# Optimization experiments

Hardware: AMD Instinct MI355X
Metric: run time of the kernel (lower is better)

Reference implementation:

```python
import jax, jax.numpy as jnp
import numpy as np

E = 256      # embedding_dim
H = 8        # num_heads
D = E // H   # head_dim = 32
F = 1024     # dim_feedforward
EPS = 1e-5


def layer_norm(x, gamma, beta):
    mu = jnp.mean(x, axis=-1, keepdims=True)
    var = jnp.var(x, axis=-1, keepdims=True)
    return (x - mu) * jax.lax.rsqrt(var + EPS) * gamma + beta


def setup_inputs() -> dict:
    key = jax.random.key(0)
    ks = jax.random.split(key, 12)
    s = lambda fan_in: 1.0 / np.sqrt(fan_in)
    src = jax.random.normal(ks[0], (4, 2048, E), dtype=jnp.float32)
    w_in = jax.random.uniform(ks[1], (3 * E, E), minval=-s(E), maxval=s(E), dtype=jnp.float32)
    w_out = jax.random.uniform(ks[2], (E, E), minval=-s(E), maxval=s(E), dtype=jnp.float32)
    w1 = jax.random.uniform(ks[3], (F, E), minval=-s(E), maxval=s(E), dtype=jnp.float32)
    b1 = jax.random.uniform(ks[4], (F,), minval=-s(E), maxval=s(E), dtype=jnp.float32)
    w2 = jax.random.uniform(ks[5], (E, F), minval=-s(F), maxval=s(F), dtype=jnp.float32)
    b2 = jax.random.uniform(ks[6], (E,), minval=-s(F), maxval=s(F), dtype=jnp.float32)
    g1 = jnp.ones((E,), jnp.float32)
    beta1 = jnp.zeros((E,), jnp.float32)
    g2 = jnp.ones((E,), jnp.float32)
    beta2 = jnp.zeros((E,), jnp.float32)
    return {"src": src, "w_in": w_in, "w_out": w_out, "w1": w1, "b1": b1,
            "w2": w2, "b2": b2, "g1": g1, "beta1": beta1, "g2": g2, "beta2": beta2}


def reference(src, w_in, w_out, w1, b1, w2, b2, g1, beta1, g2, beta2):
    B, S, _ = src.shape
    scale = D ** (-0.5)
    # --- pre-norm self-attention block ---
    x = layer_norm(src, g1, beta1)                 # [B,S,E]
    qkv = x @ w_in.T                               # [B,S,3E]
    q, k, v = jnp.split(qkv, 3, axis=-1)
    q = q.reshape(B, S, H, D).transpose(0, 2, 1, 3)  # [B,H,S,D]
    k = k.reshape(B, S, H, D).transpose(0, 2, 1, 3)
    v = v.reshape(B, S, H, D).transpose(0, 2, 1, 3)
    scores = jnp.einsum('bhqd,bhkd->bhqk', q, k) * scale  # [B,H,S,S]
    attn = jax.nn.softmax(scores, axis=-1)
    out = jnp.einsum('bhqk,bhkd->bhqd', attn, v)   # [B,H,S,D]
    out = out.transpose(0, 2, 1, 3).reshape(B, S, E)
    src = src + out @ w_out.T
    # --- pre-norm FFN block ---
    y = layer_norm(src, g2, beta2)
    y = jax.nn.relu(y @ w1.T + b1) @ w2.T + b2
    return src + y
```

## Files before the change

### kernel.cpp

```cpp
#include <hip/hip_runtime.h>
#include <hip/hip_bf16.h>
#include <math.h>

typedef unsigned short u16;
typedef unsigned int   u32;
using bf16x8 = __attribute__((ext_vector_type(8))) short;
using f32x4  = __attribute__((ext_vector_type(4))) float;

#define TE 256
#define TH 8
#define TS 2048
#define TB 4
#define NTOK 8192
#define QSCALE 0.2550120651552454f
#define EXP2(x) __builtin_amdgcn_exp2f(x)

__device__ __forceinline__ void async16(const u16* g, u16* l) {
    __builtin_amdgcn_global_load_lds(
        (const __attribute__((address_space(1))) u32*)g,
        (__attribute__((address_space(3))) u32*)l, 16, 0, 0);
}
__device__ __forceinline__ u32 pkbf(float a, float b) {
    u32 ua = __float_as_uint(a) + 0x8000u;
    u32 ub = __float_as_uint(b) + 0x8000u;
    return __builtin_amdgcn_perm(ub, ua, 0x07060302u);
}

__global__ __launch_bounds__(256) void ln_bf(const float* __restrict__ in,
        u16* __restrict__ out, const float* __restrict__ gamma,
        const float* __restrict__ beta) {
    int row  = blockIdx.x * 4 + (threadIdx.x >> 6);
    int lane = threadIdx.x & 63;
    float4 v = ((const float4*)(in + (size_t)row * TE))[lane];
    float s  = v.x + v.y + v.z + v.w;
    float s2 = v.x*v.x + v.y*v.y + v.z*v.z + v.w*v.w;
    #pragma unroll
    for (int off = 32; off > 0; off >>= 1) {
        s  += __shfl_down(s,  off, 64);
        s2 += __shfl_down(s2, off, 64);
    }
    s  = __shfl(s,  0, 64);
    s2 = __shfl(s2, 0, 64);
    float mu = s * (1.f / TE);
    float rs = rsqrtf(s2 * (1.f / TE) - mu * mu + 1e-5f);
    float4 g = ((const float4*)gamma)[lane];
    float4 b = ((const float4*)beta )[lane];
    u32 lo = pkbf((v.x - mu) * rs * g.x + b.x, (v.y - mu) * rs * g.y + b.y);
    u32 hi = pkbf((v.z - mu) * rs * g.z + b.z, (v.w - mu) * rs * g.w + b.w);
    ((uint2*)(out + (size_t)row * TE))[lane] = make_uint2(lo, hi);
}

__global__ __launch_bounds__(256) void convw(const float* __restrict__ s0, u16* d0,
        const float* __restrict__ s1, u16* d1, const float* __restrict__ s2, u16* d2,
        const float* __restrict__ s3, u16* d3) {
    int i = (blockIdx.x * 256 + threadIdx.x) * 4;
    const float* s; u16* d;
    if      (i < 196608) { s = s0; d = d0; }
    else if (i < 262144) { s = s1; d = d1; i -= 196608; }
    else if (i < 524288) { s = s2; d = d2; i -= 262144; }
    else                 { s = s3; d = d3; i -= 524288; }
    float4 v = *(const float4*)(s + i);
    *(uint2*)(d + i) = make_uint2(pkbf(v.x, v.y), pkbf(v.z, v.w));
}

template<int K, int BM, int EPI>
__global__ __launch_bounds__(256) void mgemm(const u16* __restrict__ A,
        const u16* __restrict__ W, const float* __restrict__ bias,
        const float* __restrict__ R, float* __restrict__ Cf,
        u16* __restrict__ Cb, int M) {
    constexpr int BN = BM;
    __shared__ u16 Al[2][BM * 32];
    __shared__ u16 Wl[2][BN * 32];
    const int tid = threadIdx.x, w = tid >> 6, l = tid & 63;
    const int n0 = blockIdx.y * BM;
    const int m0 = blockIdx.x * BN;
    constexpr int NT = (BM == 128) ? 4 : 2;
    constexpr int NF = (BM == 128) ? 4 : 2;
    const int tw = (w & 1) * NT * 16;
    const int fw = (w >> 1) * NF * 16;
    const int fr = l & 15, fq = l >> 4;
    const int sr = l >> 2, sc = (l & 3) * 8;
    f32x4 acc[NT][NF];
    #pragma unroll
    for (int t = 0; t < NT; t++)
        #pragma unroll
        for (int f = 0; f < NF; f++)
            #pragma unroll
            for (int r = 0; r < 4; r++) acc[t][f][r] = 0.f;

    for (int k0 = 0; k0 < K; k0 += 64) {
        __syncthreads();
        #pragma unroll
        for (int hh = 0; hh < 2; hh++) {
            const int kc = k0 + hh * 32;
            if (BM == 128) {
                #pragma unroll
                for (int c = 0; c < 2; c++) {
                    int rr = (w * 2 + c) * 16 + sr;
                    async16(A + (size_t)(n0 + rr) * K + kc + sc, &Al[hh][(w * 2 + c) * 512]);
                    async16(W + (size_t)(m0 + rr) * K + kc + sc, &Wl[hh][(w * 2 + c) * 512]);
                }
            } else {
                int rr = w * 16 + sr;
                async16(A + (size_t)(n0 + rr) * K + kc + sc, &Al[hh][w * 512]);
                async16(W + (size_t)(m0 + rr) * K + kc + sc, &Wl[hh][w * 512]);
            }
        }
        __syncthreads();
        #pragma unroll
        for (int hh = 0; hh < 2; hh++) {
            bf16x8 af[NT], wf[NF];
            #pragma unroll
            for (int t = 0; t < NT; t++)
                af[t] = *(const bf16x8*)&Al[hh][(tw + t * 16 + fr) * 32 + fq * 8];
            #pragma unroll
            for (int f = 0; f < NF; f++)
                wf[f] = *(const bf16x8*)&Wl[hh][(fw + f * 16 + fr) * 32 + fq * 8];
            #pragma unroll
            for (int t = 0; t < NT; t++)
                #pragma unroll
                for (int f = 0; f < NF; f++)
                    acc[t][f] = __builtin_amdgcn_mfma_f32_16x16x32_bf16(
                        wf[f], af[t], acc[t][f], 0, 0, 0);
        }
    }
    #pragma unroll
    for (int t = 0; t < NT; t++) {
        const int tok = n0 + tw + t * 16 + fr;
        #pragma unroll
        for (int f = 0; f < NF; f++) {
            const int fb = m0 + fw + f * 16 + fq * 4;
            f32x4 v = acc[t][f];
            if (EPI == 0) {
                const float qs = (fb < 256) ? QSCALE : 1.f;
                *(uint2*)(Cb + (size_t)tok * M + fb) =
                    make_uint2(pkbf(v[0]*qs, v[1]*qs), pkbf(v[2]*qs, v[3]*qs));
            } else if (EPI == 1) {
                float4 r4 = *(const float4*)(R + (size_t)tok * M + fb);
                *(float4*)(Cf + (size_t)tok * M + fb) =
                    make_float4(v[0]+r4.x, v[1]+r4.y, v[2]+r4.z, v[3]+r4.w);
            } else if (EPI == 2) {
                float4 b4 = *(const float4*)(bias + fb);
                *(uint2*)(Cb + (size_t)tok * M + fb) = make_uint2(
                    pkbf(fmaxf(v[0]+b4.x, 0.f), fmaxf(v[1]+b4.y, 0.f)),
                    pkbf(fmaxf(v[2]+b4.z, 0.f), fmaxf(v[3]+b4.w, 0.f)));
            } else {
                float4 b4 = *(const float4*)(bias + fb);
                float4 r4 = *(const float4*)(R + (size_t)tok * M + fb);
                *(float4*)(Cf + (size_t)tok * M + fb) = make_float4(
                    v[0]+b4.x+r4.x, v[1]+b4.y+r4.y, v[2]+b4.z+r4.z, v[3]+b4.w+r4.w);
            }
        }
    }
}

__global__ __launch_bounds__(256) void attn_k(const u16* __restrict__ qkv,
        u16* __restrict__ attn) {
    const int bh = blockIdx.x, b = bh >> 3, h = bh & 7;
    const int q0 = blockIdx.y * 64;
    const int tid = threadIdx.x, w = tid >> 6, l = tid & 63;
    const int qw = w & 1, kw = w >> 1;
    const int fr = l & 15, fq = l >> 4;
    const size_t btok = (size_t)b * TS;

    __shared__ u16 Vt[2][4 * 1296];
    __shared__ u16 Pl[4][32 * 40];

    bf16x8 qf[2];
    #pragma unroll
    for (int qs = 0; qs < 2; qs++)
        qf[qs] = *(const bf16x8*)(qkv +
            (btok + q0 + qw * 32 + qs * 16 + fr) * 768 + h * 32 + fq * 8);

    f32x4 o[2][2];
    #pragma unroll
    for (int ds = 0; ds < 2; ds++)
        #pragma unroll
        for (int qs = 0; qs < 2; qs++)
            #pragma unroll
            for (int r = 0; r < 4; r++) o[ds][qs][r] = 0.f;
    float ps[2] = {0.f, 0.f};

    u16* Pw = Pl[w];
    const int vkv = l * 2, vd0 = qw * 16;
    const u16* kbase = qkv + btok * 768 + 256 + h * 32;
    const int kvbase = kw * 1024;

    for (int it = 0; it < 8; it++) {
        const int kv0 = kvbase + it * 128;
        __syncthreads();
        {
            const u16* va = qkv + (btok + kv0 + vkv) * 768 + 512 + h * 32 + vd0;
            uint4 ra0 = *(const uint4*)va;
            uint4 ra1 = *(const uint4*)(va + 8);
            uint4 rb0 = *(const uint4*)(va + 768);
            uint4 rb1 = *(const uint4*)(va + 776);
            const u16* pa0 = (const u16*)&ra0; const u16* pa1 = (const u16*)&ra1;
            const u16* pb0 = (const u16*)&rb0; const u16* pb1 = (const u16*)&rb1;
            u16* vb_ = &Vt[kw][(vkv >> 5) * 1296 + (vkv & 31)];
            #pragma unroll
            for (int i = 0; i < 8; i++) {
                *(u32*)&vb_[(vd0 + i) * 40]     = (u32)pa0[i] | ((u32)pb0[i] << 16);
                *(u32*)&vb_[(vd0 + 8 + i) * 40] = (u32)pa1[i] | ((u32)pb1[i] << 16);
            }
        }
        __syncthreads();
        #pragma unroll
        for (int sub = 0; sub < 4; sub++) {
            const u16* krow = kbase + (size_t)(kv0 + sub * 32) * 768;
            bf16x8 kf0 = *(const bf16x8*)(krow + (size_t)fr * 768 + fq * 8);
            bf16x8 kf1 = *(const bf16x8*)(krow + (size_t)(16 + fr) * 768 + fq * 8);
            f32x4 z; z[0] = z[1] = z[2] = z[3] = 0.f;
            #pragma unroll
            for (int qs = 0; qs < 2; qs++) {
                f32x4 st0 = __builtin_amdgcn_mfma_f32_16x16x32_bf16(kf0, qf[qs], z, 0, 0, 0);
                f32x4 st1 = __builtin_amdgcn_mfma_f32_16x16x32_bf16(kf1, qf[qs], z, 0, 0, 0);
                float p0[4], p1[4];
                #pragma unroll
                for (int r = 0; r < 4; r++) { p0[r] = EXP2(st0[r]); p1[r] = EXP2(st1[r]); }
                ps[qs] += ((p0[0]+p0[1]) + (p0[2]+p0[3]))
                        + ((p1[0]+p1[1]) + (p1[2]+p1[3]));
                u16* prow = &Pw[(qs * 16 + fr) * 40];
                *(uint2*)&prow[fq * 4]      = make_uint2(pkbf(p0[0],p0[1]), pkbf(p0[2],p0[3]));
                *(uint2*)&prow[16 + fq * 4] = make_uint2(pkbf(p1[0],p1[1]), pkbf(p1[2],p1[3]));
            }
            bf16x8 pf0 = *(const bf16x8*)&Pw[fr * 40 + fq * 8];
            bf16x8 pf1 = *(const bf16x8*)&Pw[(16 + fr) * 40 + fq * 8];
            bf16x8 vf0 = *(const bf16x8*)&Vt[kw][sub * 1296 + fr * 40 + fq * 8];
            bf16x8 vf1 = *(const bf16x8*)&Vt[kw][sub * 1296 + (16 + fr) * 40 + fq * 8];
            o[0][0] = __builtin_amdgcn_mfma_f32_16x16x32_bf16(vf0, pf0, o[0][0], 0, 0, 0);
            o[0][1] = __builtin_amdgcn_mfma_f32_16x16x32_bf16(vf0, pf1, o[0][1], 0, 0, 0);
            o[1][0] = __builtin_amdgcn_mfma_f32_16x16x32_bf16(vf1, pf0, o[1][0], 0, 0, 0);
            o[1][1] = __builtin_amdgcn_mfma_f32_16x16x32_bf16(vf1, pf1, o[1][1], 0, 0, 0);
        }
    }
    #pragma unroll
    for (int qs = 0; qs < 2; qs++) {
        ps[qs] += __shfl_xor(ps[qs], 16, 64);
        ps[qs] += __shfl_xor(ps[qs], 32, 64);
    }
    __syncthreads();
    float* mrg = (float*)&Vt[0][0];
    if (kw == 1) {
        float* p = mrg + (qw * 64 + l) * 18;
        #pragma unroll
        for (int ds = 0; ds < 2; ds++)
            #pragma unroll
            for (int qs = 0; qs < 2; qs++)
                #pragma unroll
                for (int r = 0; r < 4; r++) p[ds * 8 + qs * 4 + r] = o[ds][qs][r];
        p[16] = ps[0]; p[17] = ps[1];
    }
    __syncthreads();
    if (kw == 0) {
        const float* p = mrg + (qw * 64 + l) * 18;
        #pragma unroll
        for (int ds = 0; ds < 2; ds++)
            #pragma unroll
            for (int qs = 0; qs < 2; qs++)
                #pragma unroll
                for (int r = 0; r < 4; r++) o[ds][qs][r] += p[ds * 8 + qs * 4 + r];
        ps[0] += p[16]; ps[1] += p[17];
        #pragma unroll
        for (int qs = 0; qs < 2; qs++) {
            float inv = 1.f / ps[qs];
            int tok = (int)btok + q0 + qw * 32 + qs * 16 + fr;
            #pragma unroll
            for (int ds = 0; ds < 2; ds++) {
                *(uint2*)(attn + (size_t)tok * 256 + h * 32 + ds * 16 + fq * 4) =
                    make_uint2(pkbf(o[ds][qs][0]*inv, o[ds][qs][1]*inv),
                               pkbf(o[ds][qs][2]*inv, o[ds][qs][3]*inv));
            }
        }
    }
}

extern "C" void kernel_launch(void* const* d_in, const int* in_sizes, int n_in,
                              void* d_out, int out_size, void* d_ws, size_t ws_size,
                              hipStream_t stream) {
    const float* src  = (const float*)d_in[0];
    const float* w_in = (const float*)d_in[1];
    const float* w_out= (const float*)d_in[2];
    const float* w1   = (const float*)d_in[3];
    const float* b1   = (const float*)d_in[4];
    const float* w2   = (const float*)d_in[5];
    const float* b2   = (const float*)d_in[6];
    const float* g1   = (const float*)d_in[7];
    const float* be1  = (const float*)d_in[8];
    const float* g2   = (const float*)d_in[9];
    const float* be2  = (const float*)d_in[10];
    float* out = (float*)d_out;

    u16* xb    = (u16*)d_ws;
    u16* qkvb  = xb + (size_t)NTOK * 256;
    u16* attnb = xb;
    u16* h1b   = (u16*)d_ws;
    u16* x2b   = (u16*)((char*)d_ws + (size_t)NTOK * 1024 * 2);
    u16* wib   = x2b + (size_t)NTOK * 256;
    u16* wob   = wib + 768 * 256;
    u16* w1b   = wob + 256 * 256;
    u16* w2b   = w1b + 1024 * 256;

    convw<<<768, 256, 0, stream>>>(w_in, wib, w_out, wob, w1, w1b, w2, w2b);
    ln_bf<<<NTOK / 4, 256, 0, stream>>>(src, xb, g1, be1);
    mgemm<256, 128, 0><<<dim3(6, 64), 256, 0, stream>>>(
        xb, wib, nullptr, nullptr, nullptr, qkvb, 768);
    attn_k<<<dim3(32, 32), 256, 0, stream>>>(qkvb, attnb);
    mgemm<256, 64, 1><<<dim3(4, 128), 256, 0, stream>>>(
        attnb, wob, nullptr, src, out, nullptr, 256);
    ln_bf<<<NTOK / 4, 256, 0, stream>>>(out, x2b, g2, be2);
    mgemm<256, 128, 2><<<dim3(8, 64), 256, 0, stream>>>(
        x2b, w1b, b1, nullptr, nullptr, h1b, 1024);
    mgemm<1024, 64, 3><<<dim3(4, 128), 256, 0, stream>>>(
        h1b, w2b, b2, out, out, nullptr, 256);
}
```

Baseline: 196.2 us.

## Emit V transposed from QKV GEMM and rewrite attention with 32x32 MFMA

The QKV GEMM epilogue now writes Q and K into a 512-wide buffer and scatters V into a per-head transposed [bh][d][seq] layout. This removes the in-kernel LDS transpose of V and the related barriers in attention. The attention kernel switches to 32x32x16 MFMAs and keeps P in registers through cvt_pk_bf16 and permlane32_swap instead of an LDS round trip. It also remaps the block index so that blocks sharing a head are spread across the grid. The trade-off is that the epilogue's scalar, strided 2-byte V stores are uncoalesced, which may slow the GEMM.

```diff
diff --git a/kernel.cpp b/kernel.cpp
--- a/kernel.cpp
+++ b/kernel.cpp
@@ -6,6 +6,8 @@
 typedef unsigned int   u32;
 using bf16x8 = __attribute__((ext_vector_type(8))) short;
 using f32x4  = __attribute__((ext_vector_type(4))) float;
+using f32x16 = __attribute__((ext_vector_type(16))) float;
+using u32v4  = __attribute__((ext_vector_type(4))) u32;
 
 #define TE 256
 #define TH 8
@@ -24,6 +26,9 @@
     u32 ua = __float_as_uint(a) + 0x8000u;
     u32 ub = __float_as_uint(b) + 0x8000u;
     return __builtin_amdgcn_perm(ub, ua, 0x07060302u);
+}
+__device__ __forceinline__ u16 bf1(float a) {
+    return (u16)((__float_as_uint(a) + 0x8000u) >> 16);
 }
 
 __global__ __launch_bounds__(256) void ln_bf(const float* __restrict__ in,
@@ -132,9 +137,19 @@
             const int fb = m0 + fw + f * 16 + fq * 4;
             f32x4 v = acc[t][f];
             if (EPI == 0) {
-                const float qs = (fb < 256) ? QSCALE : 1.f;
-                *(uint2*)(Cb + (size_t)tok * M + fb) =
-                    make_uint2(pkbf(v[0]*qs, v[1]*qs), pkbf(v[2]*qs, v[3]*qs));
+                if (fb < 512) {
+                    const float qs = (fb < 256) ? QSCALE : 1.f;
+                    *(uint2*)(Cb + (size_t)tok * 512 + fb) =
+                        make_uint2(pkbf(v[0]*qs, v[1]*qs), pkbf(v[2]*qs, v[3]*qs));
+                } else {
+                    const int hh = (fb - 512) >> 5, dd = (fb - 512) & 31;
+                    u16* vt = (u16*)Cf +
+                        ((size_t)((tok >> 11) * 8 + hh) * 32 + dd) * 2048 + (tok & 2047);
+                    vt[0]    = bf1(v[0]);
+                    vt[2048] = bf1(v[1]);
+                    vt[4096] = bf1(v[2]);
+                    vt[6144] = bf1(v[3]);
+                }
             } else if (EPI == 1) {
                 float4 r4 = *(const float4*)(R + (size_t)tok * M + fb);
                 *(float4*)(Cf + (size_t)tok * M + fb) =
@@ -154,124 +169,85 @@
     }
 }
 
-__global__ __launch_bounds__(256) void attn_k(const u16* __restrict__ qkv,
-        u16* __restrict__ attn) {
-    const int bh = blockIdx.x, b = bh >> 3, h = bh & 7;
-    const int q0 = blockIdx.y * 64;
+__global__ __launch_bounds__(256, 4) void attn_k(const u16* __restrict__ qk,
+        const u16* __restrict__ vt, u16* __restrict__ attn) {
+    const int id = blockIdx.x;
+    const int bh   = (id & 7) * 4 + (id >> 8);
+    const int tile = (id >> 3) & 31;
+    const int b = bh >> 3, h = bh & 7;
     const int tid = threadIdx.x, w = tid >> 6, l = tid & 63;
     const int qw = w & 1, kw = w >> 1;
-    const int fr = l & 15, fq = l >> 4;
+    const int lq = l & 31, hi = l >> 5;
     const size_t btok = (size_t)b * TS;
-
-    __shared__ u16 Vt[2][4 * 1296];
-    __shared__ u16 Pl[4][32 * 40];
-
-    bf16x8 qf[2];
-    #pragma unroll
-    for (int qs = 0; qs < 2; qs++)
-        qf[qs] = *(const bf16x8*)(qkv +
-            (btok + q0 + qw * 32 + qs * 16 + fr) * 768 + h * 32 + fq * 8);
-
-    f32x4 o[2][2];
-    #pragma unroll
-    for (int ds = 0; ds < 2; ds++)
-        #pragma unroll
-        for (int qs = 0; qs < 2; qs++)
-            #pragma unroll
-            for (int r = 0; r < 4; r++) o[ds][qs][r] = 0.f;
-    float ps[2] = {0.f, 0.f};
-
-    u16* Pw = Pl[w];
-    const int vkv = l * 2, vd0 = qw * 16;
-    const u16* kbase = qkv + btok * 768 + 256 + h * 32;
-    const int kvbase = kw * 1024;
-
-    for (int it = 0; it < 8; it++) {
-        const int kv0 = kvbase + it * 128;
-        __syncthreads();
-        {
-            const u16* va = qkv + (btok + kv0 + vkv) * 768 + 512 + h * 32 + vd0;
-            uint4 ra0 = *(const uint4*)va;
-            uint4 ra1 = *(const uint4*)(va + 8);
-            uint4 rb0 = *(const uint4*)(va + 768);
-            uint4 rb1 = *(const uint4*)(va + 776);
-            const u16* pa0 = (const u16*)&ra0; const u16* pa1 = (const u16*)&ra1;
-            const u16* pb0 = (const u16*)&rb0; const u16* pb1 = (const u16*)&rb1;
-            u16* vb_ = &Vt[kw][(vkv >> 5) * 1296 + (vkv & 31)];
-            #pragma unroll
-            for (int i = 0; i < 8; i++) {
-                *(u32*)&vb_[(vd0 + i) * 40]     = (u32)pa0[i] | ((u32)pb0[i] << 16);
-                *(u32*)&vb_[(vd0 + 8 + i) * 40] = (u32)pa1[i] | ((u32)pb1[i] << 16);
-            }
-        }
-        __syncthreads();
-        #pragma unroll
-        for (int sub = 0; sub < 4; sub++) {
-            const u16* krow = kbase + (size_t)(kv0 + sub * 32) * 768;
-            bf16x8 kf0 = *(const bf16x8*)(krow + (size_t)fr * 768 + fq * 8);
-            bf16x8 kf1 = *(const bf16x8*)(krow + (size_t)(16 + fr) * 768 + fq * 8);
-            f32x4 z; z[0] = z[1] = z[2] = z[3] = 0.f;
-            #pragma unroll
-            for (int qs = 0; qs < 2; qs++) {
-                f32x4 st0 = __builtin_amdgcn_mfma_f32_16x16x32_bf16(kf0, qf[qs], z, 0, 0, 0);
-                f32x4 st1 = __builtin_amdgcn_mfma_f32_16x16x32_bf16(kf1, qf[qs], z, 0, 0, 0);
-                float p0[4], p1[4];
-                #pragma unroll
-                for (int r = 0; r < 4; r++) { p0[r] = EXP2(st0[r]); p1[r] = EXP2(st1[r]); }
-                ps[qs] += ((p0[0]+p0[1]) + (p0[2]+p0[3]))
-                        + ((p1[0]+p1[1]) + (p1[2]+p1[3]));
-                u16* prow = &Pw[(qs * 16 + fr) * 40];
-                *(uint2*)&prow[fq * 4]      = make_uint2(pkbf(p0[0],p0[1]), pkbf(p0[2],p0[3]));
-                *(uint2*)&prow[16 + fq * 4] = make_uint2(pkbf(p1[0],p1[1]), pkbf(p1[2],p1[3]));
-            }
-            bf16x8 pf0 = *(const bf16x8*)&Pw[fr * 40 + fq * 8];
-            bf16x8 pf1 = *(const bf16x8*)&Pw[(16 + fr) * 40 + fq * 8];
-            bf16x8 vf0 = *(const bf16x8*)&Vt[kw][sub * 1296 + fr * 40 + fq * 8];
-            bf16x8 vf1 = *(const bf16x8*)&Vt[kw][sub * 1296 + (16 + fr) * 40 + fq * 8];
-            o[0][0] = __builtin_amdgcn_mfma_f32_16x16x32_bf16(vf0, pf0, o[0][0], 0, 0, 0);
-            o[0][1] = __builtin_amdgcn_mfma_f32_16x16x32_bf16(vf0, pf1, o[0][1], 0, 0, 0);
-            o[1][0] = __builtin_amdgcn_mfma_f32_16x16x32_bf16(vf1, pf0, o[1][0], 0, 0, 0);
-            o[1][1] = __builtin_amdgcn_mfma_f32_16x16x32_bf16(vf1, pf1, o[1][1], 0, 0, 0);
-        }
-    }
-    #pragma unroll
-    for (int qs = 0; qs < 2; qs++) {
-        ps[qs] += __shfl_xor(ps[qs], 16, 64);
-        ps[qs] += __shfl_xor(ps[qs], 32, 64);
-    }
-    __syncthreads();
-    float* mrg = (float*)&Vt[0][0];
+    const int q0 = tile * 64 + qw * 32;
+
+    __shared__ float mrg[2304];
+
+    const u16* qrow = qk + (btok + q0 + lq) * 512 + h * 32 + hi * 8;
+    bf16x8 qf0 = *(const bf16x8*)qrow;
+    bf16x8 qf1 = *(const bf16x8*)(qrow + 16);
+
+    const u16* kb = qk + (btok + (size_t)kw * 1024) * 512 + 256 + h * 32 + hi * 8;
+    const u16* vb = vt + ((size_t)bh * 32 + lq) * 2048 + kw * 1024 + hi * 8;
+
+    f32x16 zf, o;
+    #pragma unroll
+    for (int r = 0; r < 16; r++) { zf[r] = 0.f; o[r] = 0.f; }
+    float ps = 0.f;
+
+    u32 koff = (u32)lq * 512;
+    u32 voff = 0;
+    for (int it = 0; it < 32; ++it) {
+        bf16x8 kf0 = *(const bf16x8*)(kb + koff);
+        bf16x8 kf1 = *(const bf16x8*)(kb + koff + 16);
+        bf16x8 vf0 = *(const bf16x8*)(vb + voff);
+        bf16x8 vf1 = *(const bf16x8*)(vb + voff + 16);
+        koff += 32 * 512;
+        voff += 32;
+        f32x16 p = __builtin_amdgcn_mfma_f32_32x32x16_bf16(kf0, qf0, zf, 0, 0, 0);
+        p = __builtin_amdgcn_mfma_f32_32x32x16_bf16(kf1, qf1, p, 0, 0, 0);
+        float e[16];
+        #pragma unroll
+        for (int r = 0; r < 16; r++) e[r] = EXP2(p[r]);
+        ps += ((e[0]+e[1]) + (e[2]+e[3])) + ((e[4]+e[5]) + (e[6]+e[7]))
+            + ((e[8]+e[9]) + (e[10]+e[11])) + ((e[12]+e[13]) + (e[14]+e[15]));
+        u32 a[8];
+        #pragma unroll
+        for (int j = 0; j < 8; j++)
+            asm("v_cvt_pk_bf16_f32 %0, %1, %2"
+                : "=v"(a[j]) : "v"(e[2*j]), "v"(e[2*j+1]));
+        asm("v_permlane32_swap_b32 %0, %1" : "+v"(a[0]), "+v"(a[2]));
+        asm("v_permlane32_swap_b32 %0, %1" : "+v"(a[1]), "+v"(a[3]));
+        asm("v_permlane32_swap_b32 %0, %1" : "+v"(a[4]), "+v"(a[6]));
+        asm("v_permlane32_swap_b32 %0, %1" : "+v"(a[5]), "+v"(a[7]));
+        u32v4 t0 = {a[0], a[1], a[2], a[3]};
+        u32v4 t1 = {a[4], a[5], a[6], a[7]};
+        bf16x8 pf0 = __builtin_bit_cast(bf16x8, t0);
+        bf16x8 pf1 = __builtin_bit_cast(bf16x8, t1);
+        o = __builtin_amdgcn_mfma_f32_32x32x16_bf16(vf0, pf0, o, 0, 0, 0);
+        o = __builtin_amdgcn_mfma_f32_32x32x16_bf16(vf1, pf1, o, 0, 0, 0);
+    }
+    ps += __shfl_xor(ps, 32, 64);
+
     if (kw == 1) {
-        float* p = mrg + (qw * 64 + l) * 18;
-        #pragma unroll
-        for (int ds = 0; ds < 2; ds++)
-            #pragma unroll
-            for (int qs = 0; qs < 2; qs++)
-                #pragma unroll
-                for (int r = 0; r < 4; r++) p[ds * 8 + qs * 4 + r] = o[ds][qs][r];
-        p[16] = ps[0]; p[17] = ps[1];
+        float* d = mrg + (qw * 64 + l) * 18;
+        #pragma unroll
+        for (int r = 0; r < 16; r++) d[r] = o[r];
+        d[16] = ps;
     }
     __syncthreads();
     if (kw == 0) {
-        const float* p = mrg + (qw * 64 + l) * 18;
-        #pragma unroll
-        for (int ds = 0; ds < 2; ds++)
-            #pragma unroll
-            for (int qs = 0; qs < 2; qs++)
-                #pragma unroll
-                for (int r = 0; r < 4; r++) o[ds][qs][r] += p[ds * 8 + qs * 4 + r];
-        ps[0] += p[16]; ps[1] += p[17];
-        #pragma unroll
-        for (int qs = 0; qs < 2; qs++) {
-            float inv = 1.f / ps[qs];
-            int tok = (int)btok + q0 + qw * 32 + qs * 16 + fr;
-            #pragma unroll
-            for (int ds = 0; ds < 2; ds++) {
-                *(uint2*)(attn + (size_t)tok * 256 + h * 32 + ds * 16 + fq * 4) =
-                    make_uint2(pkbf(o[ds][qs][0]*inv, o[ds][qs][1]*inv),
-                               pkbf(o[ds][qs][2]*inv, o[ds][qs][3]*inv));
-            }
-        }
+        const float* d = mrg + (qw * 64 + l) * 18;
+        #pragma unroll
+        for (int r = 0; r < 16; r++) o[r] += d[r];
+        ps += d[16];
+        float inv = 1.f / ps;
+        int tok = (int)btok + q0 + lq;
+        u16* orow = attn + (size_t)tok * 256 + h * 32 + hi * 4;
+        #pragma unroll
+        for (int g = 0; g < 4; g++)
+            *(uint2*)(orow + g * 8) = make_uint2(
+                pkbf(o[4*g]*inv, o[4*g+1]*inv), pkbf(o[4*g+2]*inv, o[4*g+3]*inv));
     }
 }
 
@@ -292,7 +268,8 @@
     float* out = (float*)d_out;
 
     u16* xb    = (u16*)d_ws;
-    u16* qkvb  = xb + (size_t)NTOK * 256;
+    u16* qkb   = xb + (size_t)NTOK * 256;
+    u16* vtb   = qkb + (size_t)NTOK * 512;
     u16* attnb = xb;
     u16* h1b   = (u16*)d_ws;
     u16* x2b   = (u16*)((char*)d_ws + (size_t)NTOK * 1024 * 2);
@@ -304,8 +281,8 @@
     convw<<<768, 256, 0, stream>>>(w_in, wib, w_out, wob, w1, w1b, w2, w2b);
     ln_bf<<<NTOK / 4, 256, 0, stream>>>(src, xb, g1, be1);
     mgemm<256, 128, 0><<<dim3(6, 64), 256, 0, stream>>>(
-        xb, wib, nullptr, nullptr, nullptr, qkvb, 768);
-    attn_k<<<dim3(32, 32), 256, 0, stream>>>(qkvb, attnb);
+        xb, wib, nullptr, nullptr, (float*)vtb, qkb, 768);
+    attn_k<<<dim3(1024), 256, 0, stream>>>(qkb, vtb, attnb);
     mgemm<256, 64, 1><<<dim3(4, 128), 256, 0, stream>>>(
         attnb, wob, nullptr, src, out, nullptr, 256);
     ln_bf<<<NTOK / 4, 256, 0, stream>>>(out, x2b, g2, be2);
```

Result: no change. 195.2 us (-0.5%).
